# Kernel optimization log

Measured on AMD Instinct MI355X. Metric: run time of the kernel, lower is better.

Reference implementation:

```python
import jax, jax.numpy as jnp
import numpy as np

EPS_IN = 1e-4   # added to concatenated inputs before variance (as in original)
EPS_OUT = 1e-6  # added after NaN masking (as in original)


def _mdl_masked(a, b):
    """Diagonal-covariance Mahalanobis distance matrix [B,B], NaN-masked, +eps.

    Original TF code builds diag(var), inverts it with tf.linalg.inv and does two
    dense matmuls; mathematically that is an elementwise divide by the per-feature
    variance followed by diff @ diff^T, which is what we compute here.
    """
    in_co = jnp.concatenate((a, b), axis=0) + EPS_IN          # [2B, D]
    var = jnp.var(in_co, axis=0)                              # [D] per-feature variance
    diff = a - b                                              # [B, D]
    q = jnp.einsum('id,jd->ij', diff / var, diff)             # [B, B] = diff @ inv(diag(var)) @ diff^T
    # sqrt of negative entries is NaN in the original; multiply_no_nan zeroes them.
    neg = q < 0.0
    mdist = jnp.where(neg, 0.0, jnp.sqrt(jnp.where(neg, 1.0, q)))
    return mdist + EPS_OUT


def setup_inputs() -> dict:
    key = jax.random.key(0)
    k1, k2, k3 = jax.random.split(key, 3)
    B, D = 8192, 64
    return {
        'anchor': jax.random.normal(k1, (B, D), dtype=jnp.float32),
        'positive': jax.random.normal(k2, (B, D), dtype=jnp.float32),
        'negative': jax.random.normal(k3, (B, D), dtype=jnp.float32),
    }


def reference(anchor, positive, negative):
    ap = _mdl_masked(anchor, positive)   # [B, B]
    an = _mdl_masked(anchor, negative)   # [B, B]
    ap_dis = jnp.sum(ap, axis=-1)        # [B]
    ap_neg = jnp.sum(an, axis=-1)        # [B]
    return (ap_dis, ap_neg)
```

## Files before the change

kernel.cpp:

```cpp
#include <hip/hip_runtime.h>
#include <hip/hip_bf16.h>


typedef short bf16x8 __attribute__((ext_vector_type(8)));
typedef unsigned short u16x8 __attribute__((ext_vector_type(8)));
typedef float f32x4 __attribute__((ext_vector_type(4)));

#define BROWS 8192
#define DFEAT 64
#define NCO   16384
#define EPS_IN  1e-4f
#define EPS_OUT 1e-6f
#define NSTEP 32

#define WS_INVSTD 0
#define WS_EHL_F  128
#define WS_PART_F 1024
#define EHL_PAIR_USHORTS ((size_t)BROWS * 128)

static __device__ inline unsigned short f2bf_rne(float x) {
  unsigned u = __float_as_uint(x);
  unsigned r = (u + 0x7FFF + ((u >> 16) & 1)) >> 16;
  return (unsigned short)r;
}
static __device__ inline float bf2f(unsigned short s) {
  return __uint_as_float(((unsigned)s) << 16);
}

__global__ __launch_bounds__(256) void stats_kernel(
    const float* __restrict__ a, const float* __restrict__ p,
    const float* __restrict__ n, float* __restrict__ part) {
  __shared__ float acc[6][64];
  int tid = threadIdx.x;
  if (tid < 64) {
    #pragma unroll
    for (int g = 0; g < 6; ++g) acc[g][tid] = 0.f;
  }
  __syncthreads();
  int d  = tid & 63;
  int rg = tid >> 6;
  int row0 = blockIdx.x * 64;
  float sa = 0.f, qa = 0.f, sp = 0.f, qp = 0.f, sn = 0.f, qn = 0.f;
  for (int r = rg; r < 64; r += 4) {
    int idx = (row0 + r) * DFEAT + d;
    float va = a[idx] + EPS_IN; sa += va; qa += va * va;
    float vp = p[idx] + EPS_IN; sp += vp; qp += vp * vp;
    float vn = n[idx] + EPS_IN; sn += vn; qn += vn * vn;
  }
  atomicAdd(&acc[0][d], sa); atomicAdd(&acc[1][d], qa);
  atomicAdd(&acc[2][d], sp); atomicAdd(&acc[3][d], qp);
  atomicAdd(&acc[4][d], sn); atomicAdd(&acc[5][d], qn);
  __syncthreads();
  for (int v = tid; v < 384; v += 256)
    part[blockIdx.x * 384 + v] = acc[v >> 6][v & 63];
}

__global__ __launch_bounds__(256) void invstd_kernel(
    const float* __restrict__ part, float* __restrict__ inv_std) {
  __shared__ float red[4][6][64];
  int tid = threadIdx.x;
  int d = tid & 63, bg = tid >> 6;
  float s[6] = {0.f, 0.f, 0.f, 0.f, 0.f, 0.f};
  for (int b = bg; b < 128; b += 4) {
    const float* pp = part + b * 384;
    #pragma unroll
    for (int g = 0; g < 6; ++g) s[g] += pp[g * 64 + d];
  }
  #pragma unroll
  for (int g = 0; g < 6; ++g) red[bg][g][d] = s[g];
  __syncthreads();
  if (tid < 64) {
    float t[6];
    #pragma unroll
    for (int g = 0; g < 6; ++g)
      t[g] = red[0][g][d] + red[1][g][d] + red[2][g][d] + red[3][g][d];
    const float invN = 1.0f / (float)NCO;
    float m1 = (t[0] + t[2]) * invN;
    float v1 = (t[1] + t[3]) * invN - m1 * m1;
    float m2 = (t[0] + t[4]) * invN;
    float v2 = (t[1] + t[5]) * invN - m2 * m2;
    inv_std[d]      = 1.0f / sqrtf(v1);
    inv_std[64 + d] = 1.0f / sqrtf(v2);
  }
}

__global__ __launch_bounds__(256) void prep_kernel(
    const float* __restrict__ a, const float* __restrict__ p,
    const float* __restrict__ n, const float* __restrict__ inv_std,
    unsigned short* __restrict__ EHL, float* __restrict__ out) {
  __shared__ float is_s[64];
  int pair = blockIdx.x >> 8;
  int tb   = blockIdx.x & 255;
  int tid  = threadIdx.x;
  if (tid < 32) out[blockIdx.x * 32 + tid] = 0.f;
  if (tid < 64) is_s[tid] = inv_std[pair * 64 + tid];
  __syncthreads();
  const float* bptr = pair ? n : p;
  unsigned short* dst = EHL + (size_t)pair * EHL_PAIR_USHORTS;
  int c0 = tid & 7;
  int rl = tid >> 3;
  int row = tb * 32 + rl;
  int d0 = c0 * 8;
  const float* ar = a    + (size_t)row * DFEAT + d0;
  const float* br = bptr + (size_t)row * DFEAT + d0;
  float4 a0 = *(const float4*)(ar);
  float4 a1 = *(const float4*)(ar + 4);
  float4 b0 = *(const float4*)(br);
  float4 b1 = *(const float4*)(br + 4);
  float e[8] = {a0.x - b0.x, a0.y - b0.y, a0.z - b0.z, a0.w - b0.w,
                a1.x - b1.x, a1.y - b1.y, a1.z - b1.z, a1.w - b1.w};
  u16x8 vh, vl;
  #pragma unroll
  for (int j = 0; j < 8; ++j) {
    float ej = e[j] * is_s[d0 + j];
    unsigned short hi = f2bf_rne(ej);
    vh[j] = hi;
    vl[j] = f2bf_rne(ej - bf2f(hi));
  }
  int cs = c0 ^ (row & 7);
  char* drow = (char*)dst + (size_t)row * 256;
  *(u16x8*)(drow + cs * 16)       = vh;
  *(u16x8*)(drow + (8 + cs) * 16) = vl;
}

#define GLOAD(gsrc, ldst)                                                  \
  __builtin_amdgcn_global_load_lds(                                        \
      (const __attribute__((address_space(1))) void*)(gsrc),               \
      (__attribute__((address_space(3))) void*)(ldst), 16, 0, 0)

__global__ __launch_bounds__(256, 2) void mdist_mfma(
    const unsigned short* __restrict__ EHL, float* __restrict__ out) {
  __shared__ __align__(16) unsigned char sA[32768];
  __shared__ __align__(16) unsigned char sB0[16384];
  __shared__ __align__(16) unsigned char sB1[16384];
  int bid = blockIdx.x;
  int sw  = (bid & 7) * 64 + (bid >> 3);
  int pair = sw >> 8;
  int js   = (sw >> 6) & 3;
  int ib   = sw & 63;
  const char* base = (const char*)(EHL + (size_t)pair * EHL_PAIR_USHORTS);
  const char* gA = base + (size_t)ib * 32768;
  const char* gB = base + (size_t)js * (NSTEP * 16384);
  int tid = threadIdx.x;

  #pragma unroll
  for (int r = 0; r < 8; ++r) {
    int off = r * 4096 + tid * 16;
    GLOAD(gA + off, sA + off);
  }
  #pragma unroll
  for (int r = 0; r < 4; ++r) {
    int off = r * 4096 + tid * 16;
    GLOAD(gB + off, sB0 + off);
  }
  __syncthreads();

  int lane = tid & 63, w = tid >> 6;
  int wr = w >> 1, wc = w & 1;
  int l15 = lane & 15, lg = lane >> 4;

  bf16x8 af[4][4];
  #pragma unroll
  for (int hk = 0; hk < 4; ++hk) {
    int c = ((hk >> 1) << 3) | ((hk & 1) << 2) | lg;
    #pragma unroll
    for (int m = 0; m < 4; ++m) {
      int r = wr * 64 + m * 16 + l15;
      int cs = c ^ (r & 7);
      af[hk][m] = *(const bf16x8*)(sA + r * 256 + cs * 16);
    }
  }

  float rs[4][4];
  #pragma unroll
  for (int m = 0; m < 4; ++m)
    #pragma unroll
    for (int r = 0; r < 4; ++r) rs[m][r] = 0.f;

  const f32x4 zacc = {0.f, 0.f, 0.f, 0.f};
  const int AH[3] = {0, 0, 1};
  const int BH[3] = {0, 1, 0};

#define MSTEP(SBR, SBW, SIDX, DO_STAGE)                                     \
  do {                                                                      \
    if (DO_STAGE) {                                                         \
      const char* gs = gB + (SIDX) * 16384;                                 \
      _Pragma("unroll")                                                     \
      for (int r = 0; r < 4; ++r) {                                         \
        int off = r * 4096 + tid * 16;                                      \
        GLOAD(gs + off, (SBW) + off);                                       \
      }                                                                     \
    }                                                                       \
    bf16x8 bf[4][2];                                                        \
    _Pragma("unroll")                                                       \
    for (int hk = 0; hk < 4; ++hk) {                                        \
      int c = ((hk >> 1) << 3) | ((hk & 1) << 2) | lg;                      \
      _Pragma("unroll")                                                     \
      for (int nn = 0; nn < 2; ++nn) {                                      \
        int r = wc * 32 + nn * 16 + l15;                                    \
        int cs = c ^ (r & 7);                                               \
        bf[hk][nn] = *(const bf16x8*)((SBR) + r * 256 + cs * 16);           \
      }                                                                     \
    }                                                                       \
    f32x4 acc[4][2];                                                        \
    _Pragma("unroll")                                                       \
    for (int t = 0; t < 3; ++t) {                                           \
      _Pragma("unroll")                                                     \
      for (int ks = 0; ks < 2; ++ks) {                                      \
        int ahk = (AH[t] << 1) | ks;                                        \
        int bhk = (BH[t] << 1) | ks;                                        \
        _Pragma("unroll")                                                   \
        for (int m = 0; m < 4; ++m) {                                       \
          _Pragma("unroll")                                                 \
          for (int nn = 0; nn < 2; ++nn)                                    \
            acc[m][nn] = __builtin_amdgcn_mfma_f32_16x16x32_bf16(           \
                af[ahk][m], bf[bhk][nn],                                    \
                (t == 0 && ks == 0) ? zacc : acc[m][nn], 0, 0, 0);          \
        }                                                                   \
      }                                                                     \
    }                                                                       \
    _Pragma("unroll")                                                       \
    for (int m = 0; m < 4; ++m) {                                           \
      _Pragma("unroll")                                                     \
      for (int nn = 0; nn < 2; ++nn) {                                      \
        _Pragma("unroll")                                                   \
        for (int r = 0; r < 4; ++r) {                                       \
          float q = acc[m][nn][r];                                          \
          rs[m][r] += __builtin_amdgcn_sqrtf(fmaxf(q, 0.f));                \
        }                                                                   \
      }                                                                     \
    }                                                                       \
  } while (0)

  for (int ss = 0; ss < NSTEP; ss += 2) {
    MSTEP(sB0, sB1, ss + 1, true);
    __syncthreads();
    MSTEP(sB1, sB0, ss + 2, (ss + 2) < NSTEP);
    __syncthreads();
  }
#undef MSTEP

  #pragma unroll
  for (int m = 0; m < 4; ++m)
    #pragma unroll
    for (int r = 0; r < 4; ++r) {
      float v = rs[m][r];
      v += __shfl_xor(v, 1);
      v += __shfl_xor(v, 2);
      v += __shfl_xor(v, 4);
      v += __shfl_xor(v, 8);
      rs[m][r] = v;
    }
  if (l15 == 0) {
    int i0 = ib * 128;
    #pragma unroll
    for (int m = 0; m < 4; ++m)
      #pragma unroll
      for (int r = 0; r < 4; ++r)
        atomicAdd(&out[pair * BROWS + i0 + wr * 64 + m * 16 + lg * 4 + r],
                  rs[m][r] + 1024.f * EPS_OUT);
  }
}

extern "C" void kernel_launch(void* const* d_in, const int* in_sizes, int n_in,
                              void* d_out, int out_size, void* d_ws, size_t ws_size,
                              hipStream_t stream) {
  const float* anchor   = (const float*)d_in[0];
  const float* positive = (const float*)d_in[1];
  const float* negative = (const float*)d_in[2];
  float* out = (float*)d_out;
  float* ws  = (float*)d_ws;

  float* inv_std = ws + WS_INVSTD;
  float* part    = ws + WS_PART_F;
  unsigned short* EHL = (unsigned short*)(ws + WS_EHL_F);

  stats_kernel<<<128, 256, 0, stream>>>(anchor, positive, negative, part);
  invstd_kernel<<<1, 256, 0, stream>>>(part, inv_std);
  prep_kernel<<<512, 256, 0, stream>>>(anchor, positive, negative, inv_std, EHL, out);
  mdist_mfma<<<512, 256, 0, stream>>>(EHL, out);
}
```

Baseline: 129.8 us.

## Exploit symmetry of distance matrix to compute only upper-half tiles

The Gram matrix of scaled differences is symmetric, so each block now computes only half of the column tiles in a cyclic triangular schedule. Each off-diagonal tile's sqrt sums are credited to its row block and, through shuffle reductions and atomics, to its column block. The standalone variance kernel is also folded into the prep kernel, and stats accumulate with global atomics after a memset. Blocks grow to 512 threads with larger B tiles, and the extra column atomics are the added cost.

```diff
diff --git a/kernel.cpp b/kernel.cpp
--- a/kernel.cpp
+++ b/kernel.cpp
@@ -11,11 +11,8 @@
 #define NCO   16384
 #define EPS_IN  1e-4f
 #define EPS_OUT 1e-6f
-#define NSTEP 32
-
-#define WS_INVSTD 0
-#define WS_EHL_F  128
-#define WS_PART_F 1024
+
+#define WS_EHL_F 512
 #define EHL_PAIR_USHORTS ((size_t)BROWS * 128)
 
 static __device__ inline unsigned short f2bf_rne(float x) {
@@ -29,71 +26,73 @@
 
 __global__ __launch_bounds__(256) void stats_kernel(
     const float* __restrict__ a, const float* __restrict__ p,
-    const float* __restrict__ n, float* __restrict__ part) {
+    const float* __restrict__ n, float* __restrict__ stats) {
   __shared__ float acc[6][64];
   int tid = threadIdx.x;
-  if (tid < 64) {
-    #pragma unroll
-    for (int g = 0; g < 6; ++g) acc[g][tid] = 0.f;
-  }
-  __syncthreads();
-  int d  = tid & 63;
-  int rg = tid >> 6;
-  int row0 = blockIdx.x * 64;
-  float sa = 0.f, qa = 0.f, sp = 0.f, qp = 0.f, sn = 0.f, qn = 0.f;
-  for (int r = rg; r < 64; r += 4) {
-    int idx = (row0 + r) * DFEAT + d;
-    float va = a[idx] + EPS_IN; sa += va; qa += va * va;
-    float vp = p[idx] + EPS_IN; sp += vp; qp += vp * vp;
-    float vn = n[idx] + EPS_IN; sn += vn; qn += vn * vn;
-  }
-  atomicAdd(&acc[0][d], sa); atomicAdd(&acc[1][d], qa);
-  atomicAdd(&acc[2][d], sp); atomicAdd(&acc[3][d], qp);
-  atomicAdd(&acc[4][d], sn); atomicAdd(&acc[5][d], qn);
+  for (int v = tid; v < 384; v += 256) acc[v >> 6][v & 63] = 0.f;
+  __syncthreads();
+  const float4* A4 = (const float4*)a;
+  const float4* P4 = (const float4*)p;
+  const float4* N4 = (const float4*)n;
+  size_t base = (size_t)blockIdx.x * 512 + tid;
+  float s[3][4] = {}, q[3][4] = {};
+  #pragma unroll
+  for (int k = 0; k < 2; ++k) {
+    size_t idx = base + k * 256;
+    float4 va = A4[idx], vp = P4[idx], vn = N4[idx];
+    float ea[4] = {va.x, va.y, va.z, va.w};
+    float ep[4] = {vp.x, vp.y, vp.z, vp.w};
+    float en[4] = {vn.x, vn.y, vn.z, vn.w};
+    #pragma unroll
+    for (int f = 0; f < 4; ++f) {
+      float x0 = ea[f] + EPS_IN; s[0][f] += x0; q[0][f] += x0 * x0;
+      float x1 = ep[f] + EPS_IN; s[1][f] += x1; q[1][f] += x1 * x1;
+      float x2 = en[f] + EPS_IN; s[2][f] += x2; q[2][f] += x2 * x2;
+    }
+  }
+  #pragma unroll
+  for (int g = 0; g < 3; ++g)
+    #pragma unroll
+    for (int f = 0; f < 4; ++f) {
+      float vs = s[g][f], vq = q[g][f];
+      vs += __shfl_xor(vs, 16); vs += __shfl_xor(vs, 32);
+      vq += __shfl_xor(vq, 16); vq += __shfl_xor(vq, 32);
+      s[g][f] = vs; q[g][f] = vq;
+    }
+  int lane = tid & 63;
+  if (lane < 16) {
+    int d0 = lane * 4;
+    #pragma unroll
+    for (int g = 0; g < 3; ++g)
+      #pragma unroll
+      for (int f = 0; f < 4; ++f) {
+        atomicAdd(&acc[2 * g][d0 + f], s[g][f]);
+        atomicAdd(&acc[2 * g + 1][d0 + f], q[g][f]);
+      }
+  }
   __syncthreads();
   for (int v = tid; v < 384; v += 256)
-    part[blockIdx.x * 384 + v] = acc[v >> 6][v & 63];
-}
-
-__global__ __launch_bounds__(256) void invstd_kernel(
-    const float* __restrict__ part, float* __restrict__ inv_std) {
-  __shared__ float red[4][6][64];
-  int tid = threadIdx.x;
-  int d = tid & 63, bg = tid >> 6;
-  float s[6] = {0.f, 0.f, 0.f, 0.f, 0.f, 0.f};
-  for (int b = bg; b < 128; b += 4) {
-    const float* pp = part + b * 384;
-    #pragma unroll
-    for (int g = 0; g < 6; ++g) s[g] += pp[g * 64 + d];
-  }
-  #pragma unroll
-  for (int g = 0; g < 6; ++g) red[bg][g][d] = s[g];
-  __syncthreads();
-  if (tid < 64) {
-    float t[6];
-    #pragma unroll
-    for (int g = 0; g < 6; ++g)
-      t[g] = red[0][g][d] + red[1][g][d] + red[2][g][d] + red[3][g][d];
-    const float invN = 1.0f / (float)NCO;
-    float m1 = (t[0] + t[2]) * invN;
-    float v1 = (t[1] + t[3]) * invN - m1 * m1;
-    float m2 = (t[0] + t[4]) * invN;
-    float v2 = (t[1] + t[5]) * invN - m2 * m2;
-    inv_std[d]      = 1.0f / sqrtf(v1);
-    inv_std[64 + d] = 1.0f / sqrtf(v2);
-  }
+    atomicAdd(&stats[v], acc[v >> 6][v & 63]);
 }
 
 __global__ __launch_bounds__(256) void prep_kernel(
     const float* __restrict__ a, const float* __restrict__ p,
-    const float* __restrict__ n, const float* __restrict__ inv_std,
+    const float* __restrict__ n, const float* __restrict__ stats,
     unsigned short* __restrict__ EHL, float* __restrict__ out) {
   __shared__ float is_s[64];
   int pair = blockIdx.x >> 8;
   int tb   = blockIdx.x & 255;
   int tid  = threadIdx.x;
-  if (tid < 32) out[blockIdx.x * 32 + tid] = 0.f;
-  if (tid < 64) is_s[tid] = inv_std[pair * 64 + tid];
+  if (tid < 32) out[blockIdx.x * 32 + tid] = 8192.0f * EPS_OUT;
+  if (tid < 64) {
+    float sa = stats[tid], qa = stats[64 + tid];
+    float sb = pair ? stats[256 + tid] : stats[128 + tid];
+    float qb = pair ? stats[320 + tid] : stats[192 + tid];
+    const float invN = 1.0f / (float)NCO;
+    float m = (sa + sb) * invN;
+    float v = (qa + qb) * invN - m * m;
+    is_s[tid] = 1.0f / sqrtf(v);
+  }
   __syncthreads();
   const float* bptr = pair ? n : p;
   unsigned short* dst = EHL + (size_t)pair * EHL_PAIR_USHORTS;
@@ -128,35 +127,32 @@
       (const __attribute__((address_space(1))) void*)(gsrc),               \
       (__attribute__((address_space(3))) void*)(ldst), 16, 0, 0)
 
-__global__ __launch_bounds__(256, 2) void mdist_mfma(
+__global__ __launch_bounds__(512, 2) void mdist_mfma(
     const unsigned short* __restrict__ EHL, float* __restrict__ out) {
-  __shared__ __align__(16) unsigned char sA[32768];
-  __shared__ __align__(16) unsigned char sB0[16384];
-  __shared__ __align__(16) unsigned char sB1[16384];
-  int bid = blockIdx.x;
-  int sw  = (bid & 7) * 64 + (bid >> 3);
-  int pair = sw >> 8;
-  int js   = (sw >> 6) & 3;
-  int ib   = sw & 63;
+  __shared__ __align__(16) unsigned char sX[32768];
+  __shared__ __align__(16) unsigned char sY[32768];
+  int bid  = blockIdx.x;
+  int pair = bid >> 7;
+  int ib   = (bid >> 1) & 63;
+  int half = bid & 1;
   const char* base = (const char*)(EHL + (size_t)pair * EHL_PAIR_USHORTS);
   const char* gA = base + (size_t)ib * 32768;
-  const char* gB = base + (size_t)js * (NSTEP * 16384);
   int tid = threadIdx.x;
 
-  #pragma unroll
-  for (int r = 0; r < 8; ++r) {
-    int off = r * 4096 + tid * 16;
-    GLOAD(gA + off, sA + off);
-  }
-  #pragma unroll
-  for (int r = 0; r < 4; ++r) {
-    int off = r * 4096 + tid * 16;
-    GLOAD(gB + off, sB0 + off);
+  {
+    int jb0 = (ib + half) & 63;
+    const char* gB0 = base + (size_t)jb0 * 32768;
+    #pragma unroll
+    for (int r = 0; r < 4; ++r) {
+      int off = r * 8192 + tid * 16;
+      GLOAD(gA + off, sX + off);
+      GLOAD(gB0 + off, sY + off);
+    }
   }
   __syncthreads();
 
   int lane = tid & 63, w = tid >> 6;
-  int wr = w >> 1, wc = w & 1;
+  int wr = w >> 2, wc = w & 3;
   int l15 = lane & 15, lg = lane >> 4;
 
   bf16x8 af[4][4];
@@ -167,9 +163,10 @@
     for (int m = 0; m < 4; ++m) {
       int r = wr * 64 + m * 16 + l15;
       int cs = c ^ (r & 7);
-      af[hk][m] = *(const bf16x8*)(sA + r * 256 + cs * 16);
-    }
-  }
+      af[hk][m] = *(const bf16x8*)(sX + r * 256 + cs * 16);
+    }
+  }
+  __syncthreads();
 
   float rs[4][4];
   #pragma unroll
@@ -180,65 +177,82 @@
   const f32x4 zacc = {0.f, 0.f, 0.f, 0.f};
   const int AH[3] = {0, 0, 1};
   const int BH[3] = {0, 1, 0};
-
-#define MSTEP(SBR, SBW, SIDX, DO_STAGE)                                     \
-  do {                                                                      \
-    if (DO_STAGE) {                                                         \
-      const char* gs = gB + (SIDX) * 16384;                                 \
-      _Pragma("unroll")                                                     \
-      for (int r = 0; r < 4; ++r) {                                         \
-        int off = r * 4096 + tid * 16;                                      \
-        GLOAD(gs + off, (SBW) + off);                                       \
-      }                                                                     \
-    }                                                                       \
-    bf16x8 bf[4][2];                                                        \
-    _Pragma("unroll")                                                       \
-    for (int hk = 0; hk < 4; ++hk) {                                        \
-      int c = ((hk >> 1) << 3) | ((hk & 1) << 2) | lg;                      \
-      _Pragma("unroll")                                                     \
-      for (int nn = 0; nn < 2; ++nn) {                                      \
-        int r = wc * 32 + nn * 16 + l15;                                    \
-        int cs = c ^ (r & 7);                                               \
-        bf[hk][nn] = *(const bf16x8*)((SBR) + r * 256 + cs * 16);           \
-      }                                                                     \
-    }                                                                       \
-    f32x4 acc[4][2];                                                        \
-    _Pragma("unroll")                                                       \
-    for (int t = 0; t < 3; ++t) {                                           \
-      _Pragma("unroll")                                                     \
-      for (int ks = 0; ks < 2; ++ks) {                                      \
-        int ahk = (AH[t] << 1) | ks;                                        \
-        int bhk = (BH[t] << 1) | ks;                                        \
-        _Pragma("unroll")                                                   \
-        for (int m = 0; m < 4; ++m) {                                       \
-          _Pragma("unroll")                                                 \
-          for (int nn = 0; nn < 2; ++nn)                                    \
-            acc[m][nn] = __builtin_amdgcn_mfma_f32_16x16x32_bf16(           \
-                af[ahk][m], bf[bhk][nn],                                    \
-                (t == 0 && ks == 0) ? zacc : acc[m][nn], 0, 0, 0);          \
-        }                                                                   \
-      }                                                                     \
-    }                                                                       \
-    _Pragma("unroll")                                                       \
-    for (int m = 0; m < 4; ++m) {                                           \
-      _Pragma("unroll")                                                     \
-      for (int nn = 0; nn < 2; ++nn) {                                      \
-        _Pragma("unroll")                                                   \
-        for (int r = 0; r < 4; ++r) {                                       \
-          float q = acc[m][nn][r];                                          \
-          rs[m][r] += __builtin_amdgcn_sqrtf(fmaxf(q, 0.f));                \
-        }                                                                   \
-      }                                                                     \
-    }                                                                       \
-  } while (0)
-
-  for (int ss = 0; ss < NSTEP; ss += 2) {
-    MSTEP(sB0, sB1, ss + 1, true);
+  int smax = (ib < 32) ? 32 : 31;
+  int cur = 1;
+
+  for (int s = half; s <= smax; s += 2) {
+    unsigned char* wbuf = cur ? sX : sY;
+    const unsigned char* rbuf = cur ? sY : sX;
+    int snext = s + 2;
+    if (snext <= smax) {
+      int jbn = (ib + snext) & 63;
+      const char* gs = base + (size_t)jbn * 32768;
+      #pragma unroll
+      for (int r = 0; r < 4; ++r) {
+        int off = r * 8192 + tid * 16;
+        GLOAD(gs + off, wbuf + off);
+      }
+    }
+    bf16x8 bf[4][2];
+    #pragma unroll
+    for (int hk = 0; hk < 4; ++hk) {
+      int c = ((hk >> 1) << 3) | ((hk & 1) << 2) | lg;
+      #pragma unroll
+      for (int nn = 0; nn < 2; ++nn) {
+        int r = wc * 32 + nn * 16 + l15;
+        int cs = c ^ (r & 7);
+        bf[hk][nn] = *(const bf16x8*)(rbuf + r * 256 + cs * 16);
+      }
+    }
+    f32x4 acc[4][2];
+    #pragma unroll
+    for (int t = 0; t < 3; ++t) {
+      #pragma unroll
+      for (int ks = 0; ks < 2; ++ks) {
+        int ahk = (AH[t] << 1) | ks;
+        int bhk = (BH[t] << 1) | ks;
+        #pragma unroll
+        for (int m = 0; m < 4; ++m) {
+          #pragma unroll
+          for (int nn = 0; nn < 2; ++nn)
+            acc[m][nn] = __builtin_amdgcn_mfma_f32_16x16x32_bf16(
+                af[ahk][m], bf[bhk][nn],
+                (t == 0 && ks == 0) ? zacc : acc[m][nn], 0, 0, 0);
+        }
+      }
+    }
+    if (s == 0) {
+      #pragma unroll
+      for (int m = 0; m < 4; ++m)
+        #pragma unroll
+        for (int nn = 0; nn < 2; ++nn)
+          #pragma unroll
+          for (int r = 0; r < 4; ++r)
+            rs[m][r] += __builtin_amdgcn_sqrtf(fmaxf(acc[m][nn][r], 0.f));
+    } else {
+      float cq0 = 0.f, cq1 = 0.f;
+      #pragma unroll
+      for (int m = 0; m < 4; ++m)
+        #pragma unroll
+        for (int nn = 0; nn < 2; ++nn)
+          #pragma unroll
+          for (int r = 0; r < 4; ++r) {
+            float f = __builtin_amdgcn_sqrtf(fmaxf(acc[m][nn][r], 0.f));
+            rs[m][r] += f;
+            if (nn == 0) cq0 += f; else cq1 += f;
+          }
+      cq0 += __shfl_xor(cq0, 16); cq0 += __shfl_xor(cq0, 32);
+      cq1 += __shfl_xor(cq1, 16); cq1 += __shfl_xor(cq1, 32);
+      if (lane < 16) {
+        int jb = (ib + s) & 63;
+        float* orow = &out[pair * BROWS + jb * 128 + wc * 32 + l15];
+        atomicAdd(orow, cq0);
+        atomicAdd(orow + 16, cq1);
+      }
+    }
     __syncthreads();
-    MSTEP(sB1, sB0, ss + 2, (ss + 2) < NSTEP);
-    __syncthreads();
-  }
-#undef MSTEP
+    cur ^= 1;
+  }
 
   #pragma unroll
   for (int m = 0; m < 4; ++m)
@@ -252,13 +266,12 @@
       rs[m][r] = v;
     }
   if (l15 == 0) {
-    int i0 = ib * 128;
+    int i0 = ib * 128 + wr * 64;
     #pragma unroll
     for (int m = 0; m < 4; ++m)
       #pragma unroll
       for (int r = 0; r < 4; ++r)
-        atomicAdd(&out[pair * BROWS + i0 + wr * 64 + m * 16 + lg * 4 + r],
-                  rs[m][r] + 1024.f * EPS_OUT);
+        atomicAdd(&out[pair * BROWS + i0 + m * 16 + lg * 4 + r], rs[m][r]);
   }
 }
 
@@ -271,12 +284,11 @@
   float* out = (float*)d_out;
   float* ws  = (float*)d_ws;
 
-  float* inv_std = ws + WS_INVSTD;
-  float* part    = ws + WS_PART_F;
+  float* stats = ws;
   unsigned short* EHL = (unsigned short*)(ws + WS_EHL_F);
 
-  stats_kernel<<<128, 256, 0, stream>>>(anchor, positive, negative, part);
-  invstd_kernel<<<1, 256, 0, stream>>>(part, inv_std);
-  prep_kernel<<<512, 256, 0, stream>>>(anchor, positive, negative, inv_std, EHL, out);
-  mdist_mfma<<<512, 256, 0, stream>>>(EHL, out);
-}
+  hipMemsetAsync(stats, 0, 384 * sizeof(float), stream);
+  stats_kernel<<<256, 256, 0, stream>>>(anchor, positive, negative, stats);
+  prep_kernel<<<512, 256, 0, stream>>>(anchor, positive, negative, stats, EHL, out);
+  mdist_mfma<<<256, 512, 0, stream>>>(EHL, out);
+}
```

After: 108.9 us. -16.1%, faster.
